# Kernel tuning notes

Measured on AMD Instinct MI355X. Metric: run time of the kernel, lower is better.

The kernel has to match this reference:

```python
import jax, jax.numpy as jnp
import numpy as np

B, S, E, H = 1024, 200, 256, 256
C_EXPLORE = 10.0  # tanh_exploration


def setup_inputs() -> dict:
    key = jax.random.key(0)
    ks = jax.random.split(key, 19)
    rn = lambda k, shape, s=1.0: jax.random.normal(k, shape, dtype=jnp.float32) * s
    p = 0.05  # param scale to avoid tanh/sigmoid saturation
    return {
        'decoder_input': rn(ks[0], (B, E)),
        'embedded_inputs': rn(ks[1], (S, B, E)),
        'h0': rn(ks[2], (B, H)),
        'c0': rn(ks[3], (B, H)),
        'context': rn(ks[4], (S, B, H)),
        'W_ih': rn(ks[5], (4 * H, E), p), 'W_hh': rn(ks[6], (4 * H, H), p),
        'b_ih': rn(ks[7], (4 * H,), p), 'b_hh': rn(ks[8], (4 * H,), p),
        'Wq_g': rn(ks[9], (H, H), p), 'bq_g': rn(ks[10], (H,), p),
        'Wref_g': rn(ks[11], (H, H), p), 'bref_g': rn(ks[12], (H,), p),
        'v_g': rn(ks[13], (H,), p),
        'Wq_p': rn(ks[14], (H, H), p), 'bq_p': rn(ks[15], (H,), p),
        'Wref_p': rn(ks[16], (H, H), p), 'bref_p': rn(ks[17], (H,), p),
        'v_p': rn(ks[18], (H,), p),
    }


def reference(decoder_input, embedded_inputs, h0, c0, context,
              W_ih, W_hh, b_ih, b_hh,
              Wq_g, bq_g, Wref_g, bref_g, v_g,
              Wq_p, bq_p, Wref_p, bref_p, v_p):
    S_, B_ = context.shape[0], context.shape[1]
    batch_idx = jnp.arange(B_)
    neg_inf = jnp.float32(-jnp.inf)
    # 1x1-conv ref projections are constant across decode steps -> precompute [B,H,S]
    e_g = jnp.einsum('sbh,oh->bos', context, Wref_g) + bref_g[None, :, None]
    e_p = jnp.einsum('sbh,oh->bos', context, Wref_p) + bref_p[None, :, None]

    def lstm_cell(x, h, c):
        gates = x @ W_ih.T + b_ih + h @ W_hh.T + b_hh  # [B,4H], pytorch gate order i,f,g,o
        i, f, g, o = jnp.split(gates, 4, axis=1)
        c_new = jax.nn.sigmoid(f) * c + jax.nn.sigmoid(i) * jnp.tanh(g)
        h_new = jax.nn.sigmoid(o) * jnp.tanh(c_new)
        return h_new, c_new

    def attn_logits(q, e, Wq, bq, v):
        qp = q @ Wq.T + bq  # [B,H]
        return jnp.einsum('o,bos->bs', v, jnp.tanh(e + qp[:, :, None]))  # [B,S]

    def step(carry, _):
        h, c, mask, dec_in = carry
        h, c = lstm_cell(dec_in, h, c)
        # one glimpse (num_glimpses=1), mask_glimpses=True
        u = attn_logits(h, e_g, Wq_g, bq_g, v_g)
        u = jnp.where(mask, neg_inf, u)
        g_l = jnp.einsum('bos,bs->bo', e_g, jax.nn.softmax(u, axis=1))
        # pointer with tanh exploration, mask_logits=True
        u = attn_logits(g_l, e_p, Wq_p, bq_p, v_p)
        u = C_EXPLORE * jnp.tanh(u)
        u = jnp.where(mask, neg_inf, u)
        log_p = jax.nn.log_softmax(u, axis=1)  # [B,S]
        idxs = jnp.argmax(log_p, axis=1)  # greedy decode (deterministic reference)
        mask = mask.at[batch_idx, idxs].set(True)
        dec_in = embedded_inputs[idxs, batch_idx]  # gather next input [B,E]
        return (h, c, mask, dec_in), (log_p, idxs)

    mask0 = jnp.zeros((B_, S_), dtype=bool)
    (h, c, _, _), (log_ps, sels) = jax.lax.scan(
        step, (h0, c0, mask0, decoder_input), None, length=S_)
    # stack along dim=1 like torch.stack(outputs, 1)
    return jnp.transpose(log_ps, (1, 0, 2)), jnp.transpose(sels, (1, 0)), h, c
```

## Files before the change

### kernel.cpp

```cpp
#include <hip/hip_runtime.h>
#include <hip/hip_fp16.h>

static constexpr int NB = 1024;
static constexpr int NS = 200;
static constexpr int NH = 256;
static constexpr int NG4 = 1024;

#define NEG_INF (-__builtin_inff())
static constexpr float LOG2E = 1.4426950408889634f;
static constexpr float LN2   = 0.6931471805599453f;

static constexpr size_t OFF_EGS   = 0;
static constexpr size_t OFF_EPS   = OFF_EGS  + (size_t)NB*NS*NH/4;
static constexpr size_t OFF_EMBP  = OFF_EPS  + (size_t)NB*NS*NH/4;
static constexpr size_t OFF_M     = OFF_EMBP + (size_t)NS*NB*NG4/4;
static constexpr size_t OFF_WIHT  = OFF_M    + (size_t)NB*NS*NH/4;
static constexpr size_t OFF_WHHT  = OFF_WIHT + (size_t)NH*NG4;
static constexpr size_t OFF_BSUM  = OFF_WHHT + (size_t)NH*NG4;
static constexpr size_t OFF_WQG2  = OFF_BSUM + 1024;
static constexpr size_t OFF_WQTP  = OFF_WQG2 + (size_t)128*256;
static constexpr size_t OFF_WRTG  = OFF_WQTP + (size_t)NH*NH;
static constexpr size_t OFF_WRTP  = OFF_WRTG + (size_t)NH*NH;
static constexpr size_t OFF_H     = OFF_WRTP + (size_t)NH*NH;
static constexpr size_t OFF_C0    = OFF_H    + (size_t)NB*NH;
static constexpr size_t OFF_C1    = OFF_C0   + (size_t)NB*NH;
static constexpr size_t OFF_DECP0 = OFF_C1   + (size_t)NB*NH;
static constexpr size_t OFF_DECP1 = OFF_DECP0 + (size_t)NB*NG4;
static constexpr size_t OFF_WHB0  = OFF_DECP1 + (size_t)NB*NG4;
static constexpr size_t OFF_WHB1  = OFF_WHB0 + (size_t)NB*NG4;
static constexpr size_t OFF_ACT   = OFF_WHB1 + (size_t)NB*NG4;
static constexpr size_t OFF_POS   = OFF_ACT  + (size_t)NB*NS;
static constexpr size_t OFF_BPK_IH = OFF_POS + (size_t)NB*NS;
static constexpr size_t OFF_BPK_RG = OFF_BPK_IH + (size_t)32*1024*4;
static constexpr size_t OFF_BPK_RP = OFF_BPK_RG + (size_t)32*256*4;
static constexpr size_t OFF_BPK_QP = OFF_BPK_RP + (size_t)32*256*4;

static constexpr size_t OUT_SELS = (size_t)NB*NS*NS;
static constexpr size_t OUT_H    = OUT_SELS + (size_t)NB*NS;
static constexpr size_t OUT_C    = OUT_H + (size_t)NB*NH;

typedef float f32x2 __attribute__((ext_vector_type(2)));
typedef float f32x4 __attribute__((ext_vector_type(4)));
typedef short bf16x8 __attribute__((ext_vector_type(8)));

__device__ __forceinline__ float fast_exp2(float x) {
  float d; asm("v_exp_f32 %0, %1" : "=v"(d) : "v"(x)); return d;
}
__device__ __forceinline__ float fast_rcp(float x) {
  float d; asm("v_rcp_f32 %0, %1" : "=v"(d) : "v"(x)); return d;
}
__device__ __forceinline__ float fast_log2(float x) {
  float d; asm("v_log_f32 %0, %1" : "=v"(d) : "v"(x)); return d;
}
__device__ __forceinline__ float fast_tanh(float x) {
  float e = fast_exp2(x * (2.0f * LOG2E));
  return fmaf(-2.0f, fast_rcp(e + 1.0f), 1.0f);
}
__device__ __forceinline__ float fast_sigm(float x) {
  float e = fast_exp2(x * (-LOG2E));
  return fast_rcp(1.0f + e);
}
__device__ __forceinline__ float fast_expn(float a) {
  return fast_exp2(a * LOG2E);
}
__device__ __forceinline__ f32x2 cvt2_fp8(unsigned int u) {
  f32x2 d; asm("v_cvt_pk_f32_fp8 %0, %1" : "=v"(d) : "v"(u)); return d;
}
__device__ __forceinline__ unsigned int f32_to_e4m3(float x) {
  x = fminf(fmaxf(x, -448.0f), 448.0f);
  unsigned int u = __float_as_uint(x);
  unsigned int s = (u >> 24) & 0x80u;
  unsigned int au = u & 0x7fffffffu;
  if (au < 0x3c800000u) return s;
  unsigned int r = au + 0x7ffffu + ((au >> 20) & 1u);
  unsigned int expf8 = (r >> 23) - 120u;
  unsigned int man = (r >> 20) & 7u;
  return s | (expf8 << 3) | man;
}
__device__ __forceinline__ unsigned f32_bf16(float x) {
  unsigned u = __float_as_uint(x);
  unsigned r = u + 0x7fffu + ((u >> 16) & 1u);
  return r >> 16;
}

__global__ __launch_bounds__(256) void k_init(
    const float* __restrict__ h0, const float* __restrict__ c0,
    const float* __restrict__ W_ih, const float* __restrict__ W_hh,
    const float* __restrict__ b_ih, const float* __restrict__ b_hh,
    const float* __restrict__ Wq_g, const float* __restrict__ Wq_p,
    const float* __restrict__ Wref_g, const float* __restrict__ Wref_p,
    float* __restrict__ ws)
{
  const int i0 = blockIdx.x * 256 + threadIdx.x;
  const int stride = gridDim.x * 256;
  float* WIHT = ws + OFF_WIHT;
  float* WHHT = ws + OFF_WHHT;
  float* BS   = ws + OFF_BSUM;
  unsigned* WQG2 = (unsigned*)(ws + OFF_WQG2);
  for (int t = i0; t < NH * NG4; t += stride) {
    int k = t >> 10, j = t & 1023;
    int row = (j & 3) * 256 + (j >> 2);
    WIHT[t] = W_ih[row * NH + k];
    WHHT[t] = W_hh[row * NH + k];
  }
  for (int t = i0; t < 1024; t += stride) {
    int row = (t & 3) * 256 + (t >> 2);
    BS[t] = b_ih[row] + b_hh[row];
  }
  for (int t = i0; t < 128 * 256; t += stride) {
    int kk = t >> 8, o = t & 255;
    __half lo = __float2half(Wq_g[o * NH + 2 * kk]);
    __half hi = __float2half(Wq_g[o * NH + 2 * kk + 1]);
    unsigned v = ((unsigned)__half_as_ushort(hi) << 16) | (unsigned)__half_as_ushort(lo);
    WQG2[t] = v;
  }
  {
    uint4* BP = (uint4*)(ws + OFF_BPK_IH);
    for (int t = i0; t < 32 * 1024; t += stride) {
      int kg = t >> 10, n = t & 1023;
      int row = (n & 3) * 256 + (n >> 2);
      unsigned us[8];
#pragma unroll
      for (int j = 0; j < 8; ++j) us[j] = f32_bf16(W_ih[row * NH + kg * 8 + j]) & 0xffffu;
      uint4 pk = { us[0] | (us[1] << 16), us[2] | (us[3] << 16),
                   us[4] | (us[5] << 16), us[6] | (us[7] << 16) };
      BP[t] = pk;
    }
  }
  {
    uint4* BG = (uint4*)(ws + OFF_BPK_RG);
    uint4* BR = (uint4*)(ws + OFF_BPK_RP);
    uint4* BQ = (uint4*)(ws + OFF_BPK_QP);
    for (int t = i0; t < 32 * 256; t += stride) {
      int kg = t >> 8, n = t & 255;
      unsigned g[8], r[8], q[8];
#pragma unroll
      for (int j = 0; j < 8; ++j) {
        int k = kg * 8 + j;
        g[j] = f32_bf16(Wref_g[n * NH + k]) & 0xffffu;
        r[j] = f32_bf16(Wref_p[n * NH + k]) & 0xffffu;
        q[j] = f32_bf16(Wq_p[n * NH + k]) & 0xffffu;
      }
      BG[t] = (uint4){ g[0]|(g[1]<<16), g[2]|(g[3]<<16), g[4]|(g[5]<<16), g[6]|(g[7]<<16) };
      BR[t] = (uint4){ r[0]|(r[1]<<16), r[2]|(r[3]<<16), r[4]|(r[5]<<16), r[6]|(r[7]<<16) };
      BQ[t] = (uint4){ q[0]|(q[1]<<16), q[2]|(q[3]<<16), q[4]|(q[5]<<16), q[6]|(q[7]<<16) };
    }
  }
  float* hbuf = ws + OFF_H;
  float* cbuf = ws + OFF_C0;
  for (int t = i0; t < NB * NH; t += stride) {
    hbuf[t] = h0[t]; cbuf[t] = c0[t];
  }
  int* act = (int*)(ws + OFF_ACT);
  int* pos = (int*)(ws + OFF_POS);
  for (int t = i0; t < NB * NS; t += stride) {
    int s = t % NS;
    act[t] = s; pos[t] = s;
  }
}

__device__ __forceinline__ bf16x8 load_a_bf16(const float* ap) {
  float4 a0 = *(const float4*)ap;
  float4 a1 = *(const float4*)(ap + 4);
  bf16x8 af;
  af[0] = (short)f32_bf16(a0.x); af[1] = (short)f32_bf16(a0.y);
  af[2] = (short)f32_bf16(a0.z); af[3] = (short)f32_bf16(a0.w);
  af[4] = (short)f32_bf16(a1.x); af[5] = (short)f32_bf16(a1.y);
  af[6] = (short)f32_bf16(a1.z); af[7] = (short)f32_bf16(a1.w);
  return af;
}

__global__ __launch_bounds__(256) void k_embproj_mfma(
    const float* __restrict__ A, const bf16x8* __restrict__ Bpk,
    unsigned char* __restrict__ C)
{
  __shared__ float Ct[64][132];
  const int tid = threadIdx.x, l = tid & 63, w = tid >> 6;
  const int r0 = blockIdx.y * 64, n0 = blockIdx.x * 128;
  const int arow = r0 + w * 16 + (l & 15);
  const int kg0 = l >> 4;
  f32x4 acc[8] = {};
  for (int kc = 0; kc < 8; ++kc) {
    bf16x8 af = load_a_bf16(A + (size_t)arow * 256 + kc * 32 + kg0 * 8);
    const bf16x8* bp = Bpk + (size_t)(kc * 4 + kg0) * 1024 + n0 + (l & 15);
#pragma unroll
    for (int ct = 0; ct < 8; ++ct)
      acc[ct] = __builtin_amdgcn_mfma_f32_16x16x32_bf16(af, bp[ct * 16], acc[ct], 0, 0, 0);
  }
#pragma unroll
  for (int ct = 0; ct < 8; ++ct)
#pragma unroll
    for (int r = 0; r < 4; ++r)
      Ct[w * 16 + (l >> 4) * 4 + r][ct * 16 + (l & 15)] = acc[ct][r];
  __syncthreads();
  const int lr = tid >> 2, u0 = (tid & 3) * 8;
  size_t base = (size_t)(r0 + lr) * 1024 + n0;
#pragma unroll
  for (int i = 0; i < 8; ++i) {
    int cb = (u0 + i) * 4;
    unsigned pk = f32_to_e4m3(Ct[lr][cb])        | (f32_to_e4m3(Ct[lr][cb + 1]) << 8)
                | (f32_to_e4m3(Ct[lr][cb + 2]) << 16) | (f32_to_e4m3(Ct[lr][cb + 3]) << 24);
    *(unsigned*)(C + base + cb) = pk;
  }
}

__global__ __launch_bounds__(256) void k_eproj_mfma(
    const float* __restrict__ A, const bf16x8* __restrict__ Bpk,
    const float* __restrict__ bias, unsigned char* __restrict__ C)
{
  __shared__ float Ct[64][132];
  const int tid = threadIdx.x, l = tid & 63, w = tid >> 6;
  const int r0 = blockIdx.y * 64, n0 = blockIdx.x * 128;
  const int arow = r0 + w * 16 + (l & 15);
  const int kg0 = l >> 4;
  f32x4 acc[8] = {};
  for (int kc = 0; kc < 8; ++kc) {
    bf16x8 af = load_a_bf16(A + (size_t)arow * 256 + kc * 32 + kg0 * 8);
    const bf16x8* bp = Bpk + (size_t)(kc * 4 + kg0) * 256 + n0 + (l & 15);
#pragma unroll
    for (int ct = 0; ct < 8; ++ct)
      acc[ct] = __builtin_amdgcn_mfma_f32_16x16x32_bf16(af, bp[ct * 16], acc[ct], 0, 0, 0);
  }
#pragma unroll
  for (int ct = 0; ct < 8; ++ct)
#pragma unroll
    for (int r = 0; r < 4; ++r)
      Ct[w * 16 + (l >> 4) * 4 + r][ct * 16 + (l & 15)] = acc[ct][r];
  __syncthreads();
  const int lr = tid >> 2, u0 = (tid & 3) * 8;
  const int R = r0 + lr;
  const int b = R & 1023, s = R >> 10;
  size_t base = (size_t)b * (NS * NH) + (size_t)s * NH + n0;
#pragma unroll
  for (int i = 0; i < 8; ++i) {
    int cb = (u0 + i) * 4;
    unsigned pk = f32_to_e4m3(Ct[lr][cb] + bias[n0 + cb])
                | (f32_to_e4m3(Ct[lr][cb + 1] + bias[n0 + cb + 1]) << 8)
                | (f32_to_e4m3(Ct[lr][cb + 2] + bias[n0 + cb + 2]) << 16)
                | (f32_to_e4m3(Ct[lr][cb + 3] + bias[n0 + cb + 3]) << 24);
    *(unsigned*)(C + base + cb) = pk;
  }
}

__global__ __launch_bounds__(256) void k_mproj_mfma(
    const unsigned char* __restrict__ A, const bf16x8* __restrict__ Bpk,
    unsigned char* __restrict__ C)
{
  __shared__ float Ct[64][132];
  const int tid = threadIdx.x, l = tid & 63, w = tid >> 6;
  const int r0 = blockIdx.y * 64, n0 = blockIdx.x * 128;
  const int arow = r0 + w * 16 + (l & 15);
  const int kg0 = l >> 4;
  f32x4 acc[8] = {};
  for (int kc = 0; kc < 8; ++kc) {
    uint2 v = *(const uint2*)(A + (size_t)arow * 256 + kc * 32 + kg0 * 8);
    f32x2 p0 = cvt2_fp8(v.x), p1 = cvt2_fp8(v.x >> 16);
    f32x2 p2 = cvt2_fp8(v.y), p3 = cvt2_fp8(v.y >> 16);
    bf16x8 af;
    af[0] = (short)f32_bf16(p0.x); af[1] = (short)f32_bf16(p0.y);
    af[2] = (short)f32_bf16(p1.x); af[3] = (short)f32_bf16(p1.y);
    af[4] = (short)f32_bf16(p2.x); af[5] = (short)f32_bf16(p2.y);
    af[6] = (short)f32_bf16(p3.x); af[7] = (short)f32_bf16(p3.y);
    const bf16x8* bp = Bpk + (size_t)(kc * 4 + kg0) * 256 + n0 + (l & 15);
#pragma unroll
    for (int ct = 0; ct < 8; ++ct)
      acc[ct] = __builtin_amdgcn_mfma_f32_16x16x32_bf16(af, bp[ct * 16], acc[ct], 0, 0, 0);
  }
#pragma unroll
  for (int ct = 0; ct < 8; ++ct)
#pragma unroll
    for (int r = 0; r < 4; ++r)
      Ct[w * 16 + (l >> 4) * 4 + r][ct * 16 + (l & 15)] = acc[ct][r];
  __syncthreads();
  const int lr = tid >> 2, u0 = (tid & 3) * 8;
  size_t base = (size_t)(r0 + lr) * 256 + n0;
#pragma unroll
  for (int i = 0; i < 8; ++i) {
    int cb = (u0 + i) * 4;
    unsigned pk = f32_to_e4m3(Ct[lr][cb])        | (f32_to_e4m3(Ct[lr][cb + 1]) << 8)
                | (f32_to_e4m3(Ct[lr][cb + 2]) << 16) | (f32_to_e4m3(Ct[lr][cb + 3]) << 24);
    *(unsigned*)(C + base + cb) = pk;
  }
}

__global__ __launch_bounds__(256) void k_mv1024(
    const float* __restrict__ A, const float* __restrict__ WT, float* __restrict__ C)
{
  __shared__ float As[32][34];
  __shared__ float Bs[32][68];
  const int r0 = blockIdx.y * 32;
  const int n0 = blockIdx.x * 64;
  const int tid = threadIdx.x;
  const int tm = tid & 15, tn = tid >> 4;
  float acc[2][4] = {};
  for (int k0 = 0; k0 < 256; k0 += 32) {
    __syncthreads();
    {
      const int m = tid >> 3;
      const int kq = (tid & 7) * 4;
      const float* src = A + (size_t)(r0 + m) * 256 + k0 + kq;
      float4 v = *(const float4*)src;
      As[kq + 0][m] = v.x; As[kq + 1][m] = v.y; As[kq + 2][m] = v.z; As[kq + 3][m] = v.w;
    }
    {
      const int kb = tid >> 3;
      const int nq = (tid & 7) * 8;
      const float* src = WT + (size_t)(k0 + kb) * 1024 + n0 + nq;
      *(float4*)&Bs[kb][nq] = *(const float4*)src;
      *(float4*)&Bs[kb][nq + 4] = *(const float4*)(src + 4);
    }
    __syncthreads();
#pragma unroll
    for (int k = 0; k < 32; ++k) {
      float a0 = As[k][tm * 2 + 0], a1 = As[k][tm * 2 + 1];
      float4 bq = *(const float4*)&Bs[k][tn * 4];
      acc[0][0] += a0 * bq.x; acc[0][1] += a0 * bq.y; acc[0][2] += a0 * bq.z; acc[0][3] += a0 * bq.w;
      acc[1][0] += a1 * bq.x; acc[1][1] += a1 * bq.y; acc[1][2] += a1 * bq.z; acc[1][3] += a1 * bq.w;
    }
  }
#pragma unroll
  for (int i = 0; i < 2; ++i) {
    int r = r0 + tm * 2 + i;
    int j0 = n0 + tn * 4;
    float* dst = C + (size_t)r * 1024 + j0;
#pragma unroll
    for (int jj = 0; jj < 4; ++jj) dst[jj] = acc[i][jj];
  }
}

__global__ __launch_bounds__(256) void k_step(
    const unsigned char* __restrict__ egs, const unsigned char* __restrict__ eps,
    const unsigned char* __restrict__ Mbuf, const unsigned char* __restrict__ embp,
    float* __restrict__ ws,
    const float* __restrict__ bq_g, const float* __restrict__ v_g,
    const float* __restrict__ v_p, const float* __restrict__ bq_p,
    float* __restrict__ out_logp, float* __restrict__ out_sels,
    const float* __restrict__ c_in, float* __restrict__ c_out,
    const float* __restrict__ decp_in, float* __restrict__ decp_out,
    const float* __restrict__ whb_in, float* __restrict__ whb_out,
    const int t)
{
  __shared__ __align__(16) float smem[3264];
  const int blk = blockIdx.x;
  const int tid = threadIdx.x;
  const float* BS = ws + OFF_BSUM;

  if (blk >= 1024) {
    float (*As)[34] = (float(*)[34])smem;
    float (*Bs)[68] = (float(*)[68])(smem + 1088);
    const float* WHHT = ws + OFF_WHHT;
    const int mid = blk - 1024;
    const int r0 = (mid >> 4) * 32;
    const int n0 = (mid & 15) * 64;
    const int tm = tid & 15, tn = tid >> 4;
    float acc[2][4] = {};
    for (int k0 = 0; k0 < 256; k0 += 32) {
      __syncthreads();
      {
        const int m = tid >> 3;
        const int kq = (tid & 7) * 4;
        const int r = r0 + m;
        float4 c4 = *(const float4*)(c_in + (size_t)r * 256 + k0 + kq);
        float cc[4] = {c4.x, c4.y, c4.z, c4.w};
#pragma unroll
        for (int j = 0; j < 4; ++j) {
          int hc = k0 + kq + j;
          float4 dp = *(const float4*)(decp_in + (size_t)r * 1024 + hc * 4);
          float4 wh = *(const float4*)(whb_in + (size_t)r * 1024 + hc * 4);
          float4 bs = *(const float4*)(BS + hc * 4);
          float gi = dp.x + wh.x + bs.x;
          float gf = dp.y + wh.y + bs.y;
          float gg = dp.z + wh.z + bs.z;
          float go = dp.w + wh.w + bs.w;
          float cn = fast_sigm(gf) * cc[j] + fast_sigm(gi) * fast_tanh(gg);
          As[kq + j][m] = fast_sigm(go) * fast_tanh(cn);
        }
      }
      {
        const int kb = tid >> 3;
        const int nq = (tid & 7) * 8;
        const float* src = WHHT + (size_t)(k0 + kb) * 1024 + n0 + nq;
        *(float4*)&Bs[kb][nq] = *(const float4*)src;
        *(float4*)&Bs[kb][nq + 4] = *(const float4*)(src + 4);
      }
      __syncthreads();
#pragma unroll
      for (int k = 0; k < 32; ++k) {
        float a0 = As[k][tm * 2 + 0], a1 = As[k][tm * 2 + 1];
        float4 bq = *(const float4*)&Bs[k][tn * 4];
        acc[0][0] += a0 * bq.x; acc[0][1] += a0 * bq.y; acc[0][2] += a0 * bq.z; acc[0][3] += a0 * bq.w;
        acc[1][0] += a1 * bq.x; acc[1][1] += a1 * bq.y; acc[1][2] += a1 * bq.z; acc[1][3] += a1 * bq.w;
      }
    }
#pragma unroll
    for (int i = 0; i < 2; ++i) {
      int r = r0 + tm * 2 + i;
      int j0 = n0 + tn * 4;
      float* dst = whb_out + (size_t)r * 1024 + j0;
#pragma unroll
      for (int jj = 0; jj < 4; ++jj) dst[jj] = acc[i][jj];
    }
    return;
  }

  float* hs    = smem;
  float* qpg_s = smem + 256;
  float* u_s   = smem + 512;
  float* wbuf  = smem + 768;
  float* qpp_s = smem + 1024;
  int*   act_s = (int*)(smem + 1280);
  float* sred  = smem + 1480;
  float* svals = smem + 1488;
  int*   sidx  = (int*)(smem + 1496);
  int*   pick_p = (int*)(smem + 1504);

  const int b = blk;
  const int lane = tid & 63, wave = tid >> 6;
  const int nact = NS - t;
  float* h_glob = ws + OFF_H;
  const unsigned* WQG2 = (const unsigned*)(ws + OFF_WQG2);
  int* act_g = (int*)(ws + OFF_ACT);
  int* pos_g = (int*)(ws + OFF_POS);

  {
    float4 dp = *(const float4*)(decp_in + (size_t)b * 1024 + tid * 4);
    float4 wh = *(const float4*)(whb_in + (size_t)b * 1024 + tid * 4);
    float4 bs = *(const float4*)(BS + tid * 4);
    float gi = dp.x + wh.x + bs.x;
    float gf = dp.y + wh.y + bs.y;
    float gg = dp.z + wh.z + bs.z;
    float go = dp.w + wh.w + bs.w;
    float cprev = c_in[(size_t)b * 256 + tid];
    float cn = fast_sigm(gf) * cprev + fast_sigm(gi) * fast_tanh(gg);
    float hn = fast_sigm(go) * fast_tanh(cn);
    c_out[(size_t)b * 256 + tid] = cn;
    h_glob[(size_t)b * 256 + tid] = hn;
    hs[tid] = hn;
    u_s[tid] = NEG_INF;
  }
  if (tid < NS) act_s[tid] = act_g[(size_t)b * NS + tid];
  __syncthreads();

  {
    float a0 = 0.f, a1 = 0.f;
#pragma unroll 16
    for (int kk = 0; kk < 128; ++kk) {
      unsigned v = WQG2[kk * 256 + tid];
      __half2 hv = *reinterpret_cast<const __half2*>(&v);
      float2 f = __half22float2(hv);
      a0 = fmaf(hs[2 * kk], f.x, a0);
      a1 = fmaf(hs[2 * kk + 1], f.y, a1);
    }
    qpg_s[tid] = a0 + a1 + bq_g[tid];
  }
  __syncthreads();

  const unsigned char* egb = egs + (size_t)b * (NS * NH);
  const unsigned char* epb = eps + (size_t)b * (NS * NH);

  {
    float4 qv; qv.x = qpg_s[lane*4]; qv.y = qpg_s[lane*4+1]; qv.z = qpg_s[lane*4+2]; qv.w = qpg_s[lane*4+3];
    float4 vv = *(const float4*)(v_g + lane * 4);
    int j = wave;
    for (; j + 12 < nact; j += 16) {
      int s0 = act_s[j], s1 = act_s[j + 4], s2 = act_s[j + 8], s3 = act_s[j + 12];
      unsigned r0 = *(const unsigned*)(egb + (size_t)s0 * NH + 4 * lane);
      unsigned r1 = *(const unsigned*)(egb + (size_t)s1 * NH + 4 * lane);
      unsigned r2 = *(const unsigned*)(egb + (size_t)s2 * NH + 4 * lane);
      unsigned r3 = *(const unsigned*)(egb + (size_t)s3 * NH + 4 * lane);
      f32x2 a01 = cvt2_fp8(r0), a23 = cvt2_fp8(r0 >> 16);
      f32x2 b01 = cvt2_fp8(r1), b23 = cvt2_fp8(r1 >> 16);
      f32x2 c01 = cvt2_fp8(r2), c23 = cvt2_fp8(r2 >> 16);
      f32x2 d01 = cvt2_fp8(r3), d23 = cvt2_fp8(r3 >> 16);
      float t0 = vv.x * fast_tanh(a01.x + qv.x);
      t0 = fmaf(vv.y, fast_tanh(a01.y + qv.y), t0);
      t0 = fmaf(vv.z, fast_tanh(a23.x + qv.z), t0);
      t0 = fmaf(vv.w, fast_tanh(a23.y + qv.w), t0);
      float t1 = vv.x * fast_tanh(b01.x + qv.x);
      t1 = fmaf(vv.y, fast_tanh(b01.y + qv.y), t1);
      t1 = fmaf(vv.z, fast_tanh(b23.x + qv.z), t1);
      t1 = fmaf(vv.w, fast_tanh(b23.y + qv.w), t1);
      float t2 = vv.x * fast_tanh(c01.x + qv.x);
      t2 = fmaf(vv.y, fast_tanh(c01.y + qv.y), t2);
      t2 = fmaf(vv.z, fast_tanh(c23.x + qv.z), t2);
      t2 = fmaf(vv.w, fast_tanh(c23.y + qv.w), t2);
      float t3 = vv.x * fast_tanh(d01.x + qv.x);
      t3 = fmaf(vv.y, fast_tanh(d01.y + qv.y), t3);
      t3 = fmaf(vv.z, fast_tanh(d23.x + qv.z), t3);
      t3 = fmaf(vv.w, fast_tanh(d23.y + qv.w), t3);
#pragma unroll
      for (int off = 32; off; off >>= 1) {
        t0 += __shfl_xor(t0, off); t1 += __shfl_xor(t1, off);
        t2 += __shfl_xor(t2, off); t3 += __shfl_xor(t3, off);
      }
      if (lane == 0) { u_s[s0] = t0; u_s[s1] = t1; u_s[s2] = t2; u_s[s3] = t3; }
    }
    for (; j < nact; j += 4) {
      int s0 = act_s[j];
      unsigned r0 = *(const unsigned*)(egb + (size_t)s0 * NH + 4 * lane);
      f32x2 a01 = cvt2_fp8(r0), a23 = cvt2_fp8(r0 >> 16);
      float t0 = vv.x * fast_tanh(a01.x + qv.x);
      t0 = fmaf(vv.y, fast_tanh(a01.y + qv.y), t0);
      t0 = fmaf(vv.z, fast_tanh(a23.x + qv.z), t0);
      t0 = fmaf(vv.w, fast_tanh(a23.y + qv.w), t0);
#pragma unroll
      for (int off = 32; off; off >>= 1) t0 += __shfl_xor(t0, off);
      if (lane == 0) u_s[s0] = t0;
    }
  }
  __syncthreads();

  {
    float uv = (tid < NS) ? u_s[tid] : NEG_INF;
    float m = uv;
#pragma unroll
    for (int off = 32; off; off >>= 1) m = fmaxf(m, __shfl_xor(m, off));
    if (lane == 0) sred[wave] = m;
    __syncthreads();
    m = fmaxf(fmaxf(sred[0], sred[1]), fmaxf(sred[2], sred[3]));
    float ex = (uv == NEG_INF) ? 0.0f : fast_expn(uv - m);
    float sm = ex;
#pragma unroll
    for (int off = 32; off; off >>= 1) sm += __shfl_xor(sm, off);
    __syncthreads();
    if (lane == 0) sred[wave] = sm;
    __syncthreads();
    float Z = ((sred[0] + sred[1]) + sred[2]) + sred[3];
    wbuf[tid] = ex * fast_rcp(Z);
  }
  __syncthreads();

  {
    const unsigned char* Mb = Mbuf + (size_t)b * (NS * NH) + tid;
    float a0 = 0.f, a1 = 0.f, a2 = 0.f, a3 = 0.f;
    int j = 0;
    for (; j + 3 < nact; j += 4) {
      int s0 = act_s[j], s1 = act_s[j + 1], s2 = act_s[j + 2], s3 = act_s[j + 3];
      float m0 = cvt2_fp8((unsigned)Mb[(size_t)s0 * 256]).x;
      float m1 = cvt2_fp8((unsigned)Mb[(size_t)s1 * 256]).x;
      float m2 = cvt2_fp8((unsigned)Mb[(size_t)s2 * 256]).x;
      float m3 = cvt2_fp8((unsigned)Mb[(size_t)s3 * 256]).x;
      a0 = fmaf(wbuf[s0], m0, a0);
      a1 = fmaf(wbuf[s1], m1, a1);
      a2 = fmaf(wbuf[s2], m2, a2);
      a3 = fmaf(wbuf[s3], m3, a3);
    }
    for (; j < nact; ++j) {
      int s0 = act_s[j];
      a0 = fmaf(wbuf[s0], cvt2_fp8((unsigned)Mb[(size_t)s0 * 256]).x, a0);
    }
    qpp_s[tid] = ((a0 + a1) + (a2 + a3)) + bq_p[tid];
  }
  u_s[tid] = NEG_INF;
  __syncthreads();

  {
    float4 qv; qv.x = qpp_s[lane*4]; qv.y = qpp_s[lane*4+1]; qv.z = qpp_s[lane*4+2]; qv.w = qpp_s[lane*4+3];
    float4 vv = *(const float4*)(v_p + lane * 4);
    int j = wave;
    for (; j + 12 < nact; j += 16) {
      int s0 = act_s[j], s1 = act_s[j + 4], s2 = act_s[j + 8], s3 = act_s[j + 12];
      unsigned r0 = *(const unsigned*)(epb + (size_t)s0 * NH + 4 * lane);
      unsigned r1 = *(const unsigned*)(epb + (size_t)s1 * NH + 4 * lane);
      unsigned r2 = *(const unsigned*)(epb + (size_t)s2 * NH + 4 * lane);
      unsigned r3 = *(const unsigned*)(epb + (size_t)s3 * NH + 4 * lane);
      f32x2 a01 = cvt2_fp8(r0), a23 = cvt2_fp8(r0 >> 16);
      f32x2 b01 = cvt2_fp8(r1), b23 = cvt2_fp8(r1 >> 16);
      f32x2 c01 = cvt2_fp8(r2), c23 = cvt2_fp8(r2 >> 16);
      f32x2 d01 = cvt2_fp8(r3), d23 = cvt2_fp8(r3 >> 16);
      float t0 = vv.x * fast_tanh(a01.x + qv.x);
      t0 = fmaf(vv.y, fast_tanh(a01.y + qv.y), t0);
      t0 = fmaf(vv.z, fast_tanh(a23.x + qv.z), t0);
      t0 = fmaf(vv.w, fast_tanh(a23.y + qv.w), t0);
      float t1 = vv.x * fast_tanh(b01.x + qv.x);
      t1 = fmaf(vv.y, fast_tanh(b01.y + qv.y), t1);
      t1 = fmaf(vv.z, fast_tanh(b23.x + qv.z), t1);
      t1 = fmaf(vv.w, fast_tanh(b23.y + qv.w), t1);
      float t2 = vv.x * fast_tanh(c01.x + qv.x);
      t2 = fmaf(vv.y, fast_tanh(c01.y + qv.y), t2);
      t2 = fmaf(vv.z, fast_tanh(c23.x + qv.z), t2);
      t2 = fmaf(vv.w, fast_tanh(c23.y + qv.w), t2);
      float t3 = vv.x * fast_tanh(d01.x + qv.x);
      t3 = fmaf(vv.y, fast_tanh(d01.y + qv.y), t3);
      t3 = fmaf(vv.z, fast_tanh(d23.x + qv.z), t3);
      t3 = fmaf(vv.w, fast_tanh(d23.y + qv.w), t3);
#pragma unroll
      for (int off = 32; off; off >>= 1) {
        t0 += __shfl_xor(t0, off); t1 += __shfl_xor(t1, off);
        t2 += __shfl_xor(t2, off); t3 += __shfl_xor(t3, off);
      }
      if (lane == 0) {
        u_s[s0] = 10.0f * fast_tanh(t0); u_s[s1] = 10.0f * fast_tanh(t1);
        u_s[s2] = 10.0f * fast_tanh(t2); u_s[s3] = 10.0f * fast_tanh(t3);
      }
    }
    for (; j < nact; j += 4) {
      int s0 = act_s[j];
      unsigned r0 = *(const unsigned*)(epb + (size_t)s0 * NH + 4 * lane);
      f32x2 a01 = cvt2_fp8(r0), a23 = cvt2_fp8(r0 >> 16);
      float t0 = vv.x * fast_tanh(a01.x + qv.x);
      t0 = fmaf(vv.y, fast_tanh(a01.y + qv.y), t0);
      t0 = fmaf(vv.z, fast_tanh(a23.x + qv.z), t0);
      t0 = fmaf(vv.w, fast_tanh(a23.y + qv.w), t0);
#pragma unroll
      for (int off = 32; off; off >>= 1) t0 += __shfl_xor(t0, off);
      if (lane == 0) u_s[s0] = 10.0f * fast_tanh(t0);
    }
  }
  __syncthreads();

  {
    float uv = (tid < NS) ? u_s[tid] : NEG_INF;
    float m = uv;
#pragma unroll
    for (int off = 32; off; off >>= 1) m = fmaxf(m, __shfl_xor(m, off));
    if (lane == 0) sred[wave] = m;
    __syncthreads();
    m = fmaxf(fmaxf(sred[0], sred[1]), fmaxf(sred[2], sred[3]));
    float ex = (uv == NEG_INF) ? 0.0f : fast_expn(uv - m);
    float sm = ex;
#pragma unroll
    for (int off = 32; off; off >>= 1) sm += __shfl_xor(sm, off);
    __syncthreads();
    if (lane == 0) sred[wave] = sm;
    __syncthreads();
    float Z = ((sred[0] + sred[1]) + sred[2]) + sred[3];
    float lse = fast_log2(Z) * LN2;
    float lp = (uv - m) - lse;
    if (tid < NS) {
      float lp_store = fmaxf(lp, -3.0e38f);
      __builtin_nontemporal_store(lp_store,
          &out_logp[(size_t)b * (NS * NS) + (size_t)t * NS + tid]);
    }
    float av = lp; int ai = tid;
#pragma unroll
    for (int off = 32; off; off >>= 1) {
      float ov = __shfl_xor(av, off);
      int oi = __shfl_xor(ai, off);
      if (ov > av || (ov == av && oi < ai)) { av = ov; ai = oi; }
    }
    if (lane == 0) { svals[wave] = av; sidx[wave] = ai; }
    __syncthreads();
    if (tid == 0) {
      float bv = svals[0]; int bi = sidx[0];
      for (int wv = 1; wv < 4; ++wv) {
        if (svals[wv] > bv || (svals[wv] == bv && sidx[wv] < bi)) { bv = svals[wv]; bi = sidx[wv]; }
      }
      *pick_p = bi;
      __builtin_nontemporal_store((float)bi, &out_sels[(size_t)b * NS + t]);
      int j = pos_g[(size_t)b * NS + bi];
      int last = act_g[(size_t)b * NS + (nact - 1)];
      act_g[(size_t)b * NS + j] = last;
      pos_g[(size_t)b * NS + last] = j;
    }
    __syncthreads();
    const int s = *pick_p;
    const unsigned char* er = embp + ((size_t)s * NB + b) * 1024;
    unsigned v = __builtin_nontemporal_load((const unsigned*)(er + tid * 4));
    f32x2 lo = cvt2_fp8(v), hi = cvt2_fp8(v >> 16);
    float4 o4; o4.x = lo.x; o4.y = lo.y; o4.z = hi.x; o4.w = hi.y;
    *(float4*)(decp_out + (size_t)b * 1024 + tid * 4) = o4;
  }
}

__global__ __launch_bounds__(256) void k_out_hc(
    const float* __restrict__ h, const float* __restrict__ c, float* __restrict__ out)
{
  int i = blockIdx.x * 256 + threadIdx.x;
  if (i < NB * NH) {
    out[OUT_H + i] = h[i];
    out[OUT_C + i] = c[i];
  }
}

extern "C" void kernel_launch(void* const* d_in, const int* in_sizes, int n_in,
                              void* d_out, int out_size, void* d_ws, size_t ws_size,
                              hipStream_t stream)
{
  const float* dec0   = (const float*)d_in[0];
  const float* emb    = (const float*)d_in[1];
  const float* h0     = (const float*)d_in[2];
  const float* c0     = (const float*)d_in[3];
  const float* ctx    = (const float*)d_in[4];
  const float* W_ih   = (const float*)d_in[5];
  const float* W_hh   = (const float*)d_in[6];
  const float* b_ih   = (const float*)d_in[7];
  const float* b_hh   = (const float*)d_in[8];
  const float* Wq_g   = (const float*)d_in[9];
  const float* bq_g   = (const float*)d_in[10];
  const float* Wref_g = (const float*)d_in[11];
  const float* bref_g = (const float*)d_in[12];
  const float* v_g    = (const float*)d_in[13];
  const float* Wq_p   = (const float*)d_in[14];
  const float* bq_p   = (const float*)d_in[15];
  const float* Wref_p = (const float*)d_in[16];
  const float* bref_p = (const float*)d_in[17];
  const float* v_p    = (const float*)d_in[18];

  float* ws = (float*)d_ws;
  float* out = (float*)d_out;
  unsigned char* egs  = (unsigned char*)(ws + OFF_EGS);
  unsigned char* eps  = (unsigned char*)(ws + OFF_EPS);
  unsigned char* embp = (unsigned char*)(ws + OFF_EMBP);
  unsigned char* Mbuf = (unsigned char*)(ws + OFF_M);

  k_init<<<dim3(1024), dim3(256), 0, stream>>>(h0, c0, W_ih, W_hh, b_ih, b_hh,
                                               Wq_g, Wq_p, Wref_g, Wref_p, ws);
  k_eproj_mfma<<<dim3(2, 3200), dim3(256), 0, stream>>>(
      ctx, (const bf16x8*)(ws + OFF_BPK_RG), bref_g, egs);
  k_eproj_mfma<<<dim3(2, 3200), dim3(256), 0, stream>>>(
      ctx, (const bf16x8*)(ws + OFF_BPK_RP), bref_p, eps);
  k_embproj_mfma<<<dim3(8, 3200), dim3(256), 0, stream>>>(
      emb, (const bf16x8*)(ws + OFF_BPK_IH), embp);
  k_mproj_mfma<<<dim3(2, 3200), dim3(256), 0, stream>>>(
      egs, (const bf16x8*)(ws + OFF_BPK_QP), Mbuf);
  k_mv1024<<<dim3(16, 32), dim3(256), 0, stream>>>(dec0, ws + OFF_WIHT, ws + OFF_DECP0);
  k_mv1024<<<dim3(16, 32), dim3(256), 0, stream>>>(ws + OFF_H, ws + OFF_WHHT, ws + OFF_WHB0);

  for (int t = 0; t < NS; ++t) {
    const int par = t & 1;
    const float* c_in    = ws + (par ? OFF_C1 : OFF_C0);
    float*       c_outp  = ws + (par ? OFF_C0 : OFF_C1);
    const float* decp_in = ws + (par ? OFF_DECP1 : OFF_DECP0);
    float*       decp_o  = ws + (par ? OFF_DECP0 : OFF_DECP1);
    const float* whb_in  = ws + (par ? OFF_WHB1 : OFF_WHB0);
    float*       whb_o   = ws + (par ? OFF_WHB0 : OFF_WHB1);
    k_step<<<dim3(1536), dim3(256), 0, stream>>>(
        egs, eps, Mbuf, embp, ws, bq_g, v_g, v_p, bq_p,
        out, out + OUT_SELS,
        c_in, c_outp, decp_in, decp_o, whb_in, whb_o, t);
  }
  k_out_hc<<<dim3(1024), dim3(256), 0, stream>>>(ws + OFF_H, ws + OFF_C0, out);
}
```

Measured before the change: 12.61 ms.

## Store per-step gate buffers in fp8/bf16 and restructure projection GEMM kernels

Two per-step intermediates change format. The gathered input-gate projection now stays in fp8 instead of being widened to fp32, and the hidden-state gate buffer is stored as bf16. This cuts the bytes read and written by every decode step. The precompute GEMMs are rewritten so each block stages its 64 input rows once in shared memory as bf16 and loops over all output tiles, removing repeated A loads and conversions across blockIdx.x tiles. h is written to global memory only on the last step, and act/pos initialization moves to its own kernel. Lower precision of the gate inputs may change greedy argmax choices.

```diff
diff --git a/kernel.cpp b/kernel.cpp
--- a/kernel.cpp
+++ b/kernel.cpp
@@ -18,19 +18,14 @@
 static constexpr size_t OFF_WHHT  = OFF_WIHT + (size_t)NH*NG4;
 static constexpr size_t OFF_BSUM  = OFF_WHHT + (size_t)NH*NG4;
 static constexpr size_t OFF_WQG2  = OFF_BSUM + 1024;
-static constexpr size_t OFF_WQTP  = OFF_WQG2 + (size_t)128*256;
-static constexpr size_t OFF_WRTG  = OFF_WQTP + (size_t)NH*NH;
-static constexpr size_t OFF_WRTP  = OFF_WRTG + (size_t)NH*NH;
-static constexpr size_t OFF_H     = OFF_WRTP + (size_t)NH*NH;
+static constexpr size_t OFF_H     = OFF_WQG2 + (size_t)128*256;
 static constexpr size_t OFF_C0    = OFF_H    + (size_t)NB*NH;
 static constexpr size_t OFF_C1    = OFF_C0   + (size_t)NB*NH;
 static constexpr size_t OFF_DECP0 = OFF_C1   + (size_t)NB*NH;
-static constexpr size_t OFF_DECP1 = OFF_DECP0 + (size_t)NB*NG4;
-static constexpr size_t OFF_WHB0  = OFF_DECP1 + (size_t)NB*NG4;
-static constexpr size_t OFF_WHB1  = OFF_WHB0 + (size_t)NB*NG4;
-static constexpr size_t OFF_ACT   = OFF_WHB1 + (size_t)NB*NG4;
-static constexpr size_t OFF_POS   = OFF_ACT  + (size_t)NB*NS;
-static constexpr size_t OFF_BPK_IH = OFF_POS + (size_t)NB*NS;
+static constexpr size_t OFF_DECP1 = OFF_DECP0 + (size_t)NB*NG4/4;
+static constexpr size_t OFF_WHB0  = OFF_DECP1 + (size_t)NB*NG4/4;
+static constexpr size_t OFF_WHB1  = OFF_WHB0 + (size_t)NB*NG4/2;
+static constexpr size_t OFF_BPK_IH = OFF_WHB1 + (size_t)NB*NG4/2;
 static constexpr size_t OFF_BPK_RG = OFF_BPK_IH + (size_t)32*1024*4;
 static constexpr size_t OFF_BPK_RP = OFF_BPK_RG + (size_t)32*256*4;
 static constexpr size_t OFF_BPK_QP = OFF_BPK_RP + (size_t)32*256*4;
@@ -81,6 +76,9 @@
   unsigned u = __float_as_uint(x);
   unsigned r = u + 0x7fffu + ((u >> 16) & 1u);
   return r >> 16;
+}
+__device__ __forceinline__ float bf16_f32(unsigned u) {
+  return __uint_as_float(u << 16);
 }
 
 __global__ __launch_bounds__(256) void k_init(
@@ -122,9 +120,7 @@
       unsigned us[8];
 #pragma unroll
       for (int j = 0; j < 8; ++j) us[j] = f32_bf16(W_ih[row * NH + kg * 8 + j]) & 0xffffu;
-      uint4 pk = { us[0] | (us[1] << 16), us[2] | (us[3] << 16),
-                   us[4] | (us[5] << 16), us[6] | (us[7] << 16) };
-      BP[t] = pk;
+      BP[t] = (uint4){ us[0]|(us[1]<<16), us[2]|(us[3]<<16), us[4]|(us[5]<<16), us[6]|(us[7]<<16) };
     }
   }
   {
@@ -151,140 +147,132 @@
   for (int t = i0; t < NB * NH; t += stride) {
     hbuf[t] = h0[t]; cbuf[t] = c0[t];
   }
-  int* act = (int*)(ws + OFF_ACT);
-  int* pos = (int*)(ws + OFF_POS);
-  for (int t = i0; t < NB * NS; t += stride) {
-    int s = t % NS;
-    act[t] = s; pos[t] = s;
-  }
-}
-
-__device__ __forceinline__ bf16x8 load_a_bf16(const float* ap) {
-  float4 a0 = *(const float4*)ap;
-  float4 a1 = *(const float4*)(ap + 4);
-  bf16x8 af;
-  af[0] = (short)f32_bf16(a0.x); af[1] = (short)f32_bf16(a0.y);
-  af[2] = (short)f32_bf16(a0.z); af[3] = (short)f32_bf16(a0.w);
-  af[4] = (short)f32_bf16(a1.x); af[5] = (short)f32_bf16(a1.y);
-  af[6] = (short)f32_bf16(a1.z); af[7] = (short)f32_bf16(a1.w);
-  return af;
-}
-
-__global__ __launch_bounds__(256) void k_embproj_mfma(
+}
+
+
+__global__ __launch_bounds__(256) void k_embproj2(
     const float* __restrict__ A, const bf16x8* __restrict__ Bpk,
     unsigned char* __restrict__ C)
 {
-  __shared__ float Ct[64][132];
+  __shared__ unsigned short As16[64][264];
+  __shared__ float CtW[4][16][20];
   const int tid = threadIdx.x, l = tid & 63, w = tid >> 6;
-  const int r0 = blockIdx.y * 64, n0 = blockIdx.x * 128;
-  const int arow = r0 + w * 16 + (l & 15);
+  const int r0 = blockIdx.x * 64;
+#pragma unroll
+  for (int q = 0; q < 16; ++q) {
+    int idx = q * 256 + tid;
+    int row = idx >> 6, c4 = (idx & 63) * 4;
+    float4 v = *(const float4*)(A + (size_t)(r0 + row) * 256 + c4);
+    *(unsigned*)&As16[row][c4]     = f32_bf16(v.x) | (f32_bf16(v.y) << 16);
+    *(unsigned*)&As16[row][c4 + 2] = f32_bf16(v.z) | (f32_bf16(v.w) << 16);
+  }
+  __syncthreads();
+  const int arow = w * 16 + (l & 15);
   const int kg0 = l >> 4;
-  f32x4 acc[8] = {};
-  for (int kc = 0; kc < 8; ++kc) {
-    bf16x8 af = load_a_bf16(A + (size_t)arow * 256 + kc * 32 + kg0 * 8);
-    const bf16x8* bp = Bpk + (size_t)(kc * 4 + kg0) * 1024 + n0 + (l & 15);
-#pragma unroll
-    for (int ct = 0; ct < 8; ++ct)
-      acc[ct] = __builtin_amdgcn_mfma_f32_16x16x32_bf16(af, bp[ct * 16], acc[ct], 0, 0, 0);
-  }
-#pragma unroll
-  for (int ct = 0; ct < 8; ++ct)
-#pragma unroll
-    for (int r = 0; r < 4; ++r)
-      Ct[w * 16 + (l >> 4) * 4 + r][ct * 16 + (l & 15)] = acc[ct][r];
-  __syncthreads();
-  const int lr = tid >> 2, u0 = (tid & 3) * 8;
-  size_t base = (size_t)(r0 + lr) * 1024 + n0;
-#pragma unroll
-  for (int i = 0; i < 8; ++i) {
-    int cb = (u0 + i) * 4;
-    unsigned pk = f32_to_e4m3(Ct[lr][cb])        | (f32_to_e4m3(Ct[lr][cb + 1]) << 8)
-                | (f32_to_e4m3(Ct[lr][cb + 2]) << 16) | (f32_to_e4m3(Ct[lr][cb + 3]) << 24);
-    *(unsigned*)(C + base + cb) = pk;
-  }
-}
-
-__global__ __launch_bounds__(256) void k_eproj_mfma(
+  bf16x8 afr[8];
+#pragma unroll
+  for (int kc = 0; kc < 8; ++kc)
+    afr[kc] = *(const bf16x8*)&As16[arow][kc * 32 + kg0 * 8];
+  for (int ct = 0; ct < 64; ++ct) {
+    f32x4 acc = {};
+    const bf16x8* bp = Bpk + ct * 16 + (l & 15);
+#pragma unroll
+    for (int kc = 0; kc < 8; ++kc)
+      acc = __builtin_amdgcn_mfma_f32_16x16x32_bf16(afr[kc], bp[(size_t)(kc * 4 + kg0) * 1024], acc, 0, 0, 0);
+#pragma unroll
+    for (int r = 0; r < 4; ++r) CtW[w][(l >> 4) * 4 + r][l & 15] = acc[r];
+    float4 cv = *(const float4*)&CtW[w][l >> 2][(l & 3) * 4];
+    unsigned pk = f32_to_e4m3(cv.x) | (f32_to_e4m3(cv.y) << 8)
+                | (f32_to_e4m3(cv.z) << 16) | (f32_to_e4m3(cv.w) << 24);
+    *(unsigned*)(C + (size_t)(r0 + w * 16 + (l >> 2)) * 1024 + ct * 16 + (l & 3) * 4) = pk;
+  }
+}
+
+__global__ __launch_bounds__(256) void k_eproj2(
     const float* __restrict__ A, const bf16x8* __restrict__ Bpk,
     const float* __restrict__ bias, unsigned char* __restrict__ C)
 {
-  __shared__ float Ct[64][132];
+  __shared__ unsigned short As16[64][264];
+  __shared__ float CtW[4][16][20];
+  __shared__ float bias_s[256];
   const int tid = threadIdx.x, l = tid & 63, w = tid >> 6;
-  const int r0 = blockIdx.y * 64, n0 = blockIdx.x * 128;
-  const int arow = r0 + w * 16 + (l & 15);
+  const int r0 = blockIdx.x * 64;
+  bias_s[tid] = bias[tid];
+#pragma unroll
+  for (int q = 0; q < 16; ++q) {
+    int idx = q * 256 + tid;
+    int row = idx >> 6, c4 = (idx & 63) * 4;
+    float4 v = *(const float4*)(A + (size_t)(r0 + row) * 256 + c4);
+    *(unsigned*)&As16[row][c4]     = f32_bf16(v.x) | (f32_bf16(v.y) << 16);
+    *(unsigned*)&As16[row][c4 + 2] = f32_bf16(v.z) | (f32_bf16(v.w) << 16);
+  }
+  __syncthreads();
+  const int arow = w * 16 + (l & 15);
   const int kg0 = l >> 4;
-  f32x4 acc[8] = {};
-  for (int kc = 0; kc < 8; ++kc) {
-    bf16x8 af = load_a_bf16(A + (size_t)arow * 256 + kc * 32 + kg0 * 8);
-    const bf16x8* bp = Bpk + (size_t)(kc * 4 + kg0) * 256 + n0 + (l & 15);
-#pragma unroll
-    for (int ct = 0; ct < 8; ++ct)
-      acc[ct] = __builtin_amdgcn_mfma_f32_16x16x32_bf16(af, bp[ct * 16], acc[ct], 0, 0, 0);
-  }
-#pragma unroll
-  for (int ct = 0; ct < 8; ++ct)
-#pragma unroll
-    for (int r = 0; r < 4; ++r)
-      Ct[w * 16 + (l >> 4) * 4 + r][ct * 16 + (l & 15)] = acc[ct][r];
-  __syncthreads();
-  const int lr = tid >> 2, u0 = (tid & 3) * 8;
-  const int R = r0 + lr;
+  bf16x8 afr[8];
+#pragma unroll
+  for (int kc = 0; kc < 8; ++kc)
+    afr[kc] = *(const bf16x8*)&As16[arow][kc * 32 + kg0 * 8];
+  const int R = r0 + w * 16 + (l >> 2);
   const int b = R & 1023, s = R >> 10;
-  size_t base = (size_t)b * (NS * NH) + (size_t)s * NH + n0;
-#pragma unroll
-  for (int i = 0; i < 8; ++i) {
-    int cb = (u0 + i) * 4;
-    unsigned pk = f32_to_e4m3(Ct[lr][cb] + bias[n0 + cb])
-                | (f32_to_e4m3(Ct[lr][cb + 1] + bias[n0 + cb + 1]) << 8)
-                | (f32_to_e4m3(Ct[lr][cb + 2] + bias[n0 + cb + 2]) << 16)
-                | (f32_to_e4m3(Ct[lr][cb + 3] + bias[n0 + cb + 3]) << 24);
-    *(unsigned*)(C + base + cb) = pk;
-  }
-}
-
-__global__ __launch_bounds__(256) void k_mproj_mfma(
+  for (int ct = 0; ct < 16; ++ct) {
+    f32x4 acc = {};
+    const bf16x8* bp = Bpk + ct * 16 + (l & 15);
+#pragma unroll
+    for (int kc = 0; kc < 8; ++kc)
+      acc = __builtin_amdgcn_mfma_f32_16x16x32_bf16(afr[kc], bp[(size_t)(kc * 4 + kg0) * 256], acc, 0, 0, 0);
+#pragma unroll
+    for (int r = 0; r < 4; ++r) CtW[w][(l >> 4) * 4 + r][l & 15] = acc[r];
+    float4 cv = *(const float4*)&CtW[w][l >> 2][(l & 3) * 4];
+    int cb = ct * 16 + (l & 3) * 4;
+    unsigned pk = f32_to_e4m3(cv.x + bias_s[cb])       | (f32_to_e4m3(cv.y + bias_s[cb + 1]) << 8)
+                | (f32_to_e4m3(cv.z + bias_s[cb + 2]) << 16) | (f32_to_e4m3(cv.w + bias_s[cb + 3]) << 24);
+    *(unsigned*)(C + (size_t)b * (NS * NH) + (size_t)s * NH + cb) = pk;
+  }
+}
+
+__global__ __launch_bounds__(256) void k_mproj2(
     const unsigned char* __restrict__ A, const bf16x8* __restrict__ Bpk,
     unsigned char* __restrict__ C)
 {
-  __shared__ float Ct[64][132];
+  __shared__ unsigned short As16[64][264];
+  __shared__ float CtW[4][16][20];
   const int tid = threadIdx.x, l = tid & 63, w = tid >> 6;
-  const int r0 = blockIdx.y * 64, n0 = blockIdx.x * 128;
-  const int arow = r0 + w * 16 + (l & 15);
+  const int r0 = blockIdx.x * 64;
+#pragma unroll
+  for (int q = 0; q < 16; ++q) {
+    int idx = q * 256 + tid;
+    int row = idx >> 6, c4 = (idx & 63) * 4;
+    unsigned v = *(const unsigned*)(A + (size_t)(r0 + row) * 256 + c4);
+    f32x2 lo = cvt2_fp8(v), hi = cvt2_fp8(v >> 16);
+    *(unsigned*)&As16[row][c4]     = f32_bf16(lo.x) | (f32_bf16(lo.y) << 16);
+    *(unsigned*)&As16[row][c4 + 2] = f32_bf16(hi.x) | (f32_bf16(hi.y) << 16);
+  }
+  __syncthreads();
+  const int arow = w * 16 + (l & 15);
   const int kg0 = l >> 4;
-  f32x4 acc[8] = {};
-  for (int kc = 0; kc < 8; ++kc) {
-    uint2 v = *(const uint2*)(A + (size_t)arow * 256 + kc * 32 + kg0 * 8);
-    f32x2 p0 = cvt2_fp8(v.x), p1 = cvt2_fp8(v.x >> 16);
-    f32x2 p2 = cvt2_fp8(v.y), p3 = cvt2_fp8(v.y >> 16);
-    bf16x8 af;
-    af[0] = (short)f32_bf16(p0.x); af[1] = (short)f32_bf16(p0.y);
-    af[2] = (short)f32_bf16(p1.x); af[3] = (short)f32_bf16(p1.y);
-    af[4] = (short)f32_bf16(p2.x); af[5] = (short)f32_bf16(p2.y);
-    af[6] = (short)f32_bf16(p3.x); af[7] = (short)f32_bf16(p3.y);
-    const bf16x8* bp = Bpk + (size_t)(kc * 4 + kg0) * 256 + n0 + (l & 15);
-#pragma unroll
-    for (int ct = 0; ct < 8; ++ct)
-      acc[ct] = __builtin_amdgcn_mfma_f32_16x16x32_bf16(af, bp[ct * 16], acc[ct], 0, 0, 0);
-  }
-#pragma unroll
-  for (int ct = 0; ct < 8; ++ct)
-#pragma unroll
-    for (int r = 0; r < 4; ++r)
-      Ct[w * 16 + (l >> 4) * 4 + r][ct * 16 + (l & 15)] = acc[ct][r];
-  __syncthreads();
-  const int lr = tid >> 2, u0 = (tid & 3) * 8;
-  size_t base = (size_t)(r0 + lr) * 256 + n0;
-#pragma unroll
-  for (int i = 0; i < 8; ++i) {
-    int cb = (u0 + i) * 4;
-    unsigned pk = f32_to_e4m3(Ct[lr][cb])        | (f32_to_e4m3(Ct[lr][cb + 1]) << 8)
-                | (f32_to_e4m3(Ct[lr][cb + 2]) << 16) | (f32_to_e4m3(Ct[lr][cb + 3]) << 24);
-    *(unsigned*)(C + base + cb) = pk;
-  }
-}
-
-__global__ __launch_bounds__(256) void k_mv1024(
-    const float* __restrict__ A, const float* __restrict__ WT, float* __restrict__ C)
+  bf16x8 afr[8];
+#pragma unroll
+  for (int kc = 0; kc < 8; ++kc)
+    afr[kc] = *(const bf16x8*)&As16[arow][kc * 32 + kg0 * 8];
+  for (int ct = 0; ct < 16; ++ct) {
+    f32x4 acc = {};
+    const bf16x8* bp = Bpk + ct * 16 + (l & 15);
+#pragma unroll
+    for (int kc = 0; kc < 8; ++kc)
+      acc = __builtin_amdgcn_mfma_f32_16x16x32_bf16(afr[kc], bp[(size_t)(kc * 4 + kg0) * 256], acc, 0, 0, 0);
+#pragma unroll
+    for (int r = 0; r < 4; ++r) CtW[w][(l >> 4) * 4 + r][l & 15] = acc[r];
+    float4 cv = *(const float4*)&CtW[w][l >> 2][(l & 3) * 4];
+    unsigned pk = f32_to_e4m3(cv.x) | (f32_to_e4m3(cv.y) << 8)
+                | (f32_to_e4m3(cv.z) << 16) | (f32_to_e4m3(cv.w) << 24);
+    *(unsigned*)(C + (size_t)(r0 + w * 16 + (l >> 2)) * 256 + ct * 16 + (l & 3) * 4) = pk;
+  }
+}
+
+template <int MODE>
+__global__ __launch_bounds__(256) void k_mv1024t(
+    const float* __restrict__ A, const float* __restrict__ WT, void* __restrict__ Cv)
 {
   __shared__ float As[32][34];
   __shared__ float Bs[32][68];
@@ -322,9 +310,16 @@
   for (int i = 0; i < 2; ++i) {
     int r = r0 + tm * 2 + i;
     int j0 = n0 + tn * 4;
-    float* dst = C + (size_t)r * 1024 + j0;
-#pragma unroll
-    for (int jj = 0; jj < 4; ++jj) dst[jj] = acc[i][jj];
+    if (MODE == 1) {
+      unsigned pk = f32_to_e4m3(acc[i][0]) | (f32_to_e4m3(acc[i][1]) << 8)
+                  | (f32_to_e4m3(acc[i][2]) << 16) | (f32_to_e4m3(acc[i][3]) << 24);
+      ((unsigned*)Cv)[(size_t)r * 256 + (j0 >> 2)] = pk;
+    } else {
+      uint2 pk;
+      pk.x = f32_bf16(acc[i][0]) | (f32_bf16(acc[i][1]) << 16);
+      pk.y = f32_bf16(acc[i][2]) | (f32_bf16(acc[i][3]) << 16);
+      *(uint2*)((unsigned short*)Cv + (size_t)r * 1024 + j0) = pk;
+    }
   }
 }
 
@@ -336,8 +331,9 @@
     const float* __restrict__ v_p, const float* __restrict__ bq_p,
     float* __restrict__ out_logp, float* __restrict__ out_sels,
     const float* __restrict__ c_in, float* __restrict__ c_out,
-    const float* __restrict__ decp_in, float* __restrict__ decp_out,
-    const float* __restrict__ whb_in, float* __restrict__ whb_out,
+    const unsigned char* __restrict__ decp_in, unsigned char* __restrict__ decp_out,
+    const unsigned short* __restrict__ whb_in, unsigned short* __restrict__ whb_out,
+    int* __restrict__ act_g, int* __restrict__ pos_g,
     const int t)
 {
   __shared__ __align__(16) float smem[3264];
@@ -365,13 +361,14 @@
 #pragma unroll
         for (int j = 0; j < 4; ++j) {
           int hc = k0 + kq + j;
-          float4 dp = *(const float4*)(decp_in + (size_t)r * 1024 + hc * 4);
-          float4 wh = *(const float4*)(whb_in + (size_t)r * 1024 + hc * 4);
+          unsigned dpu = *(const unsigned*)(decp_in + (size_t)r * 1024 + hc * 4);
+          f32x2 d01 = cvt2_fp8(dpu), d23 = cvt2_fp8(dpu >> 16);
+          uint2 whu = *(const uint2*)(whb_in + (size_t)r * 1024 + hc * 4);
           float4 bs = *(const float4*)(BS + hc * 4);
-          float gi = dp.x + wh.x + bs.x;
-          float gf = dp.y + wh.y + bs.y;
-          float gg = dp.z + wh.z + bs.z;
-          float go = dp.w + wh.w + bs.w;
+          float gi = d01.x + bf16_f32(whu.x & 0xffffu) + bs.x;
+          float gf = d01.y + bf16_f32(whu.x >> 16) + bs.y;
+          float gg = d23.x + bf16_f32(whu.y & 0xffffu) + bs.z;
+          float go = d23.y + bf16_f32(whu.y >> 16) + bs.w;
           float cn = fast_sigm(gf) * cc[j] + fast_sigm(gi) * fast_tanh(gg);
           As[kq + j][m] = fast_sigm(go) * fast_tanh(cn);
         }
@@ -396,9 +393,10 @@
     for (int i = 0; i < 2; ++i) {
       int r = r0 + tm * 2 + i;
       int j0 = n0 + tn * 4;
-      float* dst = whb_out + (size_t)r * 1024 + j0;
-#pragma unroll
-      for (int jj = 0; jj < 4; ++jj) dst[jj] = acc[i][jj];
+      uint2 pk;
+      pk.x = f32_bf16(acc[i][0]) | (f32_bf16(acc[i][1]) << 16);
+      pk.y = f32_bf16(acc[i][2]) | (f32_bf16(acc[i][3]) << 16);
+      *(uint2*)(whb_out + (size_t)r * 1024 + j0) = pk;
     }
     return;
   }
@@ -419,22 +417,21 @@
   const int nact = NS - t;
   float* h_glob = ws + OFF_H;
   const unsigned* WQG2 = (const unsigned*)(ws + OFF_WQG2);
-  int* act_g = (int*)(ws + OFF_ACT);
-  int* pos_g = (int*)(ws + OFF_POS);
-
-  {
-    float4 dp = *(const float4*)(decp_in + (size_t)b * 1024 + tid * 4);
-    float4 wh = *(const float4*)(whb_in + (size_t)b * 1024 + tid * 4);
+
+  {
+    unsigned dpu = *(const unsigned*)(decp_in + (size_t)b * 1024 + tid * 4);
+    f32x2 d01 = cvt2_fp8(dpu), d23 = cvt2_fp8(dpu >> 16);
+    uint2 whu = *(const uint2*)(whb_in + (size_t)b * 1024 + tid * 4);
     float4 bs = *(const float4*)(BS + tid * 4);
-    float gi = dp.x + wh.x + bs.x;
-    float gf = dp.y + wh.y + bs.y;
-    float gg = dp.z + wh.z + bs.z;
-    float go = dp.w + wh.w + bs.w;
+    float gi = d01.x + bf16_f32(whu.x & 0xffffu) + bs.x;
+    float gf = d01.y + bf16_f32(whu.x >> 16) + bs.y;
+    float gg = d23.x + bf16_f32(whu.y & 0xffffu) + bs.z;
+    float go = d23.y + bf16_f32(whu.y >> 16) + bs.w;
     float cprev = c_in[(size_t)b * 256 + tid];
     float cn = fast_sigm(gf) * cprev + fast_sigm(gi) * fast_tanh(gg);
     float hn = fast_sigm(go) * fast_tanh(cn);
     c_out[(size_t)b * 256 + tid] = cn;
-    h_glob[(size_t)b * 256 + tid] = hn;
+    if (t == NS - 1) h_glob[(size_t)b * 256 + tid] = hn;
     hs[tid] = hn;
     u_s[tid] = NEG_INF;
   }
@@ -657,9 +654,16 @@
     const int s = *pick_p;
     const unsigned char* er = embp + ((size_t)s * NB + b) * 1024;
     unsigned v = __builtin_nontemporal_load((const unsigned*)(er + tid * 4));
-    f32x2 lo = cvt2_fp8(v), hi = cvt2_fp8(v >> 16);
-    float4 o4; o4.x = lo.x; o4.y = lo.y; o4.z = hi.x; o4.w = hi.y;
-    *(float4*)(decp_out + (size_t)b * 1024 + tid * 4) = o4;
+    *(unsigned*)(decp_out + (size_t)b * 1024 + tid * 4) = v;
+  }
+}
+
+__global__ __launch_bounds__(256) void k_actinit(int* __restrict__ act, int* __restrict__ pos)
+{
+  int i = blockIdx.x * 256 + threadIdx.x;
+  if (i < NB * NS) {
+    int s = i % NS;
+    act[i] = s; pos[i] = s;
   }
 }
 
@@ -703,32 +707,39 @@
   unsigned char* eps  = (unsigned char*)(ws + OFF_EPS);
   unsigned char* embp = (unsigned char*)(ws + OFF_EMBP);
   unsigned char* Mbuf = (unsigned char*)(ws + OFF_M);
+  static constexpr size_t OFF_ACT = OFF_BPK_QP + (size_t)32*256*4;
+  static constexpr size_t OFF_POS = OFF_ACT + (size_t)NB*NS;
+  int* act = (int*)(ws + OFF_ACT);
+  int* pos = (int*)(ws + OFF_POS);
 
   k_init<<<dim3(1024), dim3(256), 0, stream>>>(h0, c0, W_ih, W_hh, b_ih, b_hh,
                                                Wq_g, Wq_p, Wref_g, Wref_p, ws);
-  k_eproj_mfma<<<dim3(2, 3200), dim3(256), 0, stream>>>(
+  k_actinit<<<dim3((NB * NS + 255) / 256), dim3(256), 0, stream>>>(act, pos);
+  k_eproj2<<<dim3(3200), dim3(256), 0, stream>>>(
       ctx, (const bf16x8*)(ws + OFF_BPK_RG), bref_g, egs);
-  k_eproj_mfma<<<dim3(2, 3200), dim3(256), 0, stream>>>(
+  k_eproj2<<<dim3(3200), dim3(256), 0, stream>>>(
       ctx, (const bf16x8*)(ws + OFF_BPK_RP), bref_p, eps);
-  k_embproj_mfma<<<dim3(8, 3200), dim3(256), 0, stream>>>(
+  k_embproj2<<<dim3(3200), dim3(256), 0, stream>>>(
       emb, (const bf16x8*)(ws + OFF_BPK_IH), embp);
-  k_mproj_mfma<<<dim3(2, 3200), dim3(256), 0, stream>>>(
+  k_mproj2<<<dim3(3200), dim3(256), 0, stream>>>(
       egs, (const bf16x8*)(ws + OFF_BPK_QP), Mbuf);
-  k_mv1024<<<dim3(16, 32), dim3(256), 0, stream>>>(dec0, ws + OFF_WIHT, ws + OFF_DECP0);
-  k_mv1024<<<dim3(16, 32), dim3(256), 0, stream>>>(ws + OFF_H, ws + OFF_WHHT, ws + OFF_WHB0);
+  k_mv1024t<1><<<dim3(16, 32), dim3(256), 0, stream>>>(
+      dec0, ws + OFF_WIHT, (void*)(ws + OFF_DECP0));
+  k_mv1024t<2><<<dim3(16, 32), dim3(256), 0, stream>>>(
+      ws + OFF_H, ws + OFF_WHHT, (void*)(ws + OFF_WHB0));
 
   for (int t = 0; t < NS; ++t) {
     const int par = t & 1;
     const float* c_in    = ws + (par ? OFF_C1 : OFF_C0);
     float*       c_outp  = ws + (par ? OFF_C0 : OFF_C1);
-    const float* decp_in = ws + (par ? OFF_DECP1 : OFF_DECP0);
-    float*       decp_o  = ws + (par ? OFF_DECP0 : OFF_DECP1);
-    const float* whb_in  = ws + (par ? OFF_WHB1 : OFF_WHB0);
-    float*       whb_o   = ws + (par ? OFF_WHB0 : OFF_WHB1);
+    const unsigned char* decp_in = (const unsigned char*)(ws + (par ? OFF_DECP1 : OFF_DECP0));
+    unsigned char*       decp_o  = (unsigned char*)(ws + (par ? OFF_DECP0 : OFF_DECP1));
+    const unsigned short* whb_in = (const unsigned short*)(ws + (par ? OFF_WHB1 : OFF_WHB0));
+    unsigned short*       whb_o  = (unsigned short*)(ws + (par ? OFF_WHB0 : OFF_WHB1));
     k_step<<<dim3(1536), dim3(256), 0, stream>>>(
         egs, eps, Mbuf, embp, ws, bq_g, v_g, v_p, bq_p,
         out, out + OUT_SELS,
-        c_in, c_outp, decp_in, decp_o, whb_in, whb_o, t);
+        c_in, c_outp, decp_in, decp_o, whb_in, whb_o, act, pos, t);
   }
   k_out_hc<<<dim3(1024), dim3(256), 0, stream>>>(ws + OFF_H, ws + OFF_C0, out);
 }
```

Result: faster. 11.10 ms (-11.9%).
